# Kernel tuning notes

Hardware: AMD Instinct MI355X
Metric: run time of the kernel (lower is better)

## Reference

```python
import jax, jax.numpy as jnp
import numpy as np

B, S, HID = 2, 2048, 2048
NH, NKV, HD = 16, 8, 128
GROUPS = NH // NKV
EPS = 1e-6
SCALE = HD ** -0.5
ROPE_THETA = 1000000.0


def _rope_cos_sin(seq_len, head_dim, batch):
    inv_freq = 1.0 / (ROPE_THETA ** (np.arange(0, head_dim, 2, dtype=np.float32) / head_dim))
    t = np.arange(seq_len, dtype=np.float32)
    freqs = np.outer(t, inv_freq)                      # [S, HD/2]
    emb = np.concatenate([freqs, freqs], axis=-1)      # [S, HD]
    cos = np.broadcast_to(np.cos(emb), (batch, seq_len, head_dim))
    sin = np.broadcast_to(np.sin(emb), (batch, seq_len, head_dim))
    return jnp.asarray(cos), jnp.asarray(sin)


def setup_inputs() -> dict:
    key = jax.random.key(0)
    ks = jax.random.split(key, 6)
    hidden_states = jax.random.normal(ks[0], (B, S, HID), dtype=jnp.float32)
    cos, sin = _rope_cos_sin(S, HD, B)
    w_scale = HID ** -0.5
    Wq = jax.random.normal(ks[1], (NH * HD, HID), dtype=jnp.float32) * w_scale
    Wk = jax.random.normal(ks[2], (NKV * HD, HID), dtype=jnp.float32) * w_scale
    Wv = jax.random.normal(ks[3], (NKV * HD, HID), dtype=jnp.float32) * w_scale
    Wo = jax.random.normal(ks[4], (HID, NH * HD), dtype=jnp.float32) * w_scale
    q_norm_w = jnp.ones((HD,), dtype=jnp.float32)
    k_norm_w = jnp.ones((HD,), dtype=jnp.float32)
    return {"hidden_states": hidden_states, "cos": cos, "sin": sin,
            "Wq": Wq, "Wk": Wk, "Wv": Wv, "Wo": Wo,
            "q_norm_w": q_norm_w, "k_norm_w": k_norm_w}


def _rms_norm(x, w):
    # RMSNorm over last dim (head_dim), variance computed in fp32
    var = jnp.mean(x.astype(jnp.float32) ** 2, axis=-1, keepdims=True)
    return w * (x * jax.lax.rsqrt(var + EPS).astype(x.dtype))


def _rotate_half(x):
    x1, x2 = jnp.split(x, 2, axis=-1)
    return jnp.concatenate([-x2, x1], axis=-1)


def _apply_rope(x, cos, sin):
    # x: [B, H, S, D]; cos/sin: [B, S, D] -> unsqueeze head dim
    c = cos[:, None, :, :]
    s = sin[:, None, :, :]
    return x * c + _rotate_half(x) * s


def reference(hidden_states, cos, sin, Wq, Wk, Wv, Wo, q_norm_w, k_norm_w):
    b, s, _ = hidden_states.shape
    # QKV projections (bias=False per config.attention_bias)
    q = (hidden_states @ Wq.T).reshape(b, s, NH, HD)
    k = (hidden_states @ Wk.T).reshape(b, s, NKV, HD)
    v = (hidden_states @ Wv.T).reshape(b, s, NKV, HD)
    # Per-head QK RMSNorm, then [B, H, S, D]
    q = _rms_norm(q, q_norm_w).transpose(0, 2, 1, 3)
    k = _rms_norm(k, k_norm_w).transpose(0, 2, 1, 3)
    v = v.transpose(0, 2, 1, 3)
    # RoPE
    q = _apply_rope(q, cos, sin)
    k = _apply_rope(k, cos, sin)
    # GQA: expand kv heads to match query heads
    k = jnp.repeat(k, GROUPS, axis=1)
    v = jnp.repeat(v, GROUPS, axis=1)
    # SDPA (is_causal=False, mask=None, dropout=0)
    scores = jnp.einsum('bhqd,bhkd->bhqk', q, k) * SCALE
    probs = jax.nn.softmax(scores, axis=-1)
    attn = jnp.einsum('bhqk,bhkd->bhqd', probs, v)
    attn = attn.transpose(0, 2, 1, 3).reshape(b, s, NH * HD)
    return attn @ Wo.T
```

## Files before the change

kernel.cpp:

```cpp
#include <hip/hip_runtime.h>

using short8 = __attribute__((ext_vector_type(8))) short;
using f32x4  = __attribute__((ext_vector_type(4))) float;
using u32x2  = __attribute__((ext_vector_type(2))) unsigned int;
using u32x4  = __attribute__((ext_vector_type(4))) unsigned int;

#define MFMA16(a, b, c) __builtin_amdgcn_mfma_f32_16x16x32_bf16((a), (b), (c), 0, 0, 0)

__device__ inline float bf2f(ushort v) { return __uint_as_float(((unsigned int)v) << 16); }
__device__ inline unsigned int f2bfu(float f) {
  unsigned int u = __float_as_uint(f);
  return (u + 0x7fffu + ((u >> 16) & 1u)) >> 16;
}
__device__ inline unsigned int pk2(float a, float b) { return f2bfu(a) | (f2bfu(b) << 16); }
__device__ inline unsigned int pk2hw(float lo, float hi) {
  unsigned int r;
  asm("v_cvt_pk_bf16_f32 %0, %1, %2" : "=v"(r) : "v"(lo), "v"(hi));
  return r;
}

__device__ inline void gl_lds16(const ushort* g, ushort* l) {
  __builtin_amdgcn_global_load_lds(
      (const __attribute__((address_space(1))) void*)g,
      (__attribute__((address_space(3))) void*)l, 16, 0, 0);
}

__global__ __launch_bounds__(256) void f2b8(const float* __restrict__ src,
                                            ushort* __restrict__ dst, int n) {
  int i = (blockIdx.x * 256 + threadIdx.x) * 8;
  if (i >= n) return;
  f32x4 a = *(const f32x4*)(src + i);
  f32x4 b = *(const f32x4*)(src + i + 4);
  u32x4 o;
  o[0] = pk2(a[0], a[1]); o[1] = pk2(a[2], a[3]);
  o[2] = pk2(b[0], b[1]); o[3] = pk2(b[2], b[3]);
  *(u32x4*)(dst + i) = o;
}

__global__ __launch_bounds__(256) void wconv(const float* __restrict__ Wq,
                                             const float* __restrict__ Wk,
                                             const float* __restrict__ Wv,
                                             const float* __restrict__ Wo,
                                             ushort* __restrict__ Wcomb,
                                             ushort* __restrict__ Wob) {
  int blk = blockIdx.x;
  const float* src; ushort* dst; int off;
  if (blk < 2048)      { src = Wq; dst = Wcomb;           off = blk * 2048; }
  else if (blk < 3072) { src = Wk; dst = Wcomb + 4194304; off = (blk - 2048) * 2048; }
  else if (blk < 4096) { src = Wv; dst = Wcomb + 6291456; off = (blk - 3072) * 2048; }
  else                 { src = Wo; dst = Wob;             off = (blk - 4096) * 2048; }
  int i = off + threadIdx.x * 8;
  f32x4 a = *(const f32x4*)(src + i);
  f32x4 b = *(const f32x4*)(src + i + 4);
  u32x4 o;
  o[0] = pk2(a[0], a[1]); o[1] = pk2(a[2], a[3]);
  o[2] = pk2(b[0], b[1]); o[3] = pk2(b[2], b[3]);
  *(u32x4*)(dst + i) = o;
}

#define GPHASE(CB, P, STG, VMW)                                                     \
  {                                                                                 \
    if (P == 0) {                                                                   \
      _Pragma("unroll") for (int n = 0; n < 4; ++n) {                               \
        bf[n][0] = *(const short8*)&L[(CB)*32768 + bBase + n*1024 + rdoff];         \
        bf[n][1] = *(const short8*)&L[(CB)*32768 + bBase + n*1024 + (rdoff ^ 32)];  \
      }                                                                             \
    }                                                                               \
    short8 af[2][2];                                                                \
    _Pragma("unroll") for (int mi = 0; mi < 2; ++mi) {                              \
      af[mi][0] = *(const short8*)&L[(CB)*32768 + aBase + ((P)*2+mi)*1024 + rdoff];        \
      af[mi][1] = *(const short8*)&L[(CB)*32768 + aBase + ((P)*2+mi)*1024 + (rdoff ^ 32)]; \
    }                                                                               \
    STG;                                                                            \
    __builtin_amdgcn_s_barrier();                                                   \
    asm volatile("s_waitcnt lgkmcnt(0)" ::: "memory");                              \
    __builtin_amdgcn_s_setprio(1);                                                  \
    _Pragma("unroll") for (int mi = 0; mi < 2; ++mi)                                \
      _Pragma("unroll") for (int n = 0; n < 4; ++n) {                               \
        acc[(P)*2+mi][n] = MFMA16(af[mi][0], bf[n][0], acc[(P)*2+mi][n]);           \
        acc[(P)*2+mi][n] = MFMA16(af[mi][1], bf[n][1], acc[(P)*2+mi][n]);           \
      }                                                                             \
    __builtin_amdgcn_s_setprio(0);                                                  \
    VMW;                                                                            \
    __builtin_amdgcn_s_barrier();                                                   \
  }

#define VM4 asm volatile("s_waitcnt vmcnt(4)" ::: "memory")
#define NOPX (void)0

template <int OUTF32>
__global__ __launch_bounds__(512, 2) void gemm256(const ushort* __restrict__ A,
                                                  const ushort* __restrict__ B,
                                                  void* __restrict__ Cv,
                                                  int M, int N, int K) {
  __shared__ ushort L[65536];
  const int t = threadIdx.x;
  const int w = t >> 6, l = t & 63, lr = l & 15, lg = l >> 4;
  const int wr = w >> 2, wc = w & 3;
  const int m0 = blockIdx.x * 256, n0 = blockIdx.y * 256;
  const int NT = K >> 6, NI = NT >> 1;

  f32x4 acc[8][4] = {};

  const int rdoff = lr * 64 + ((lg ^ (lr & 7)) * 8);
  const int aBase = wr * 8192;
  const int bBase = 16384 + (wc >> 1) * 8192 + (wc & 1) * 4096;

  const int ch0 = w * 2, ch1 = w * 2 + 1;
  const int srow0 = ch0 * 8 + (l >> 3), srow1 = ch1 * 8 + (l >> 3);
  const int scol = ((l & 7) ^ (l >> 3)) * 8;

  auto stage_a = [&](int h, int kt, int cb) {
    int ktc = kt < NT ? kt : NT - 1;
    gl_lds16(A + (size_t)(m0 + h * 128 + srow0) * K + ktc * 64 + scol,
             (ushort*)&L[cb * 32768 + h * 8192 + ch0 * 512]);
    gl_lds16(A + (size_t)(m0 + h * 128 + srow1) * K + ktc * 64 + scol,
             (ushort*)&L[cb * 32768 + h * 8192 + ch1 * 512]);
  };
  auto stage_b = [&](int h, int kt, int cb) {
    int ktc = kt < NT ? kt : NT - 1;
    gl_lds16(B + (size_t)(n0 + h * 128 + srow0) * K + ktc * 64 + scol,
             (ushort*)&L[cb * 32768 + 16384 + h * 8192 + ch0 * 512]);
    gl_lds16(B + (size_t)(n0 + h * 128 + srow1) * K + ktc * 64 + scol,
             (ushort*)&L[cb * 32768 + 16384 + h * 8192 + ch1 * 512]);
  };

  stage_a(0, 0, 0); stage_a(1, 0, 0); stage_b(0, 0, 0); stage_b(1, 0, 0);
  stage_b(0, 1, 1); stage_b(1, 1, 1);
  VM4;
  __builtin_amdgcn_s_barrier();

  short8 bf[4][2];
  for (int I = 0; I < NI; ++I) {
    const int t1 = 2 * I + 1, t2 = 2 * I + 2, t3 = 2 * I + 3;
    GPHASE(0, 0, stage_a(0, t1, 1), NOPX)
    GPHASE(0, 1, stage_a(1, t1, 1), NOPX)
    GPHASE(0, 2, stage_b(0, t2, 0), NOPX)
    GPHASE(0, 3, stage_b(1, t2, 0), VM4)
    GPHASE(1, 0, stage_a(0, t2, 0), NOPX)
    GPHASE(1, 1, stage_a(1, t2, 0), NOPX)
    GPHASE(1, 2, stage_b(0, t3, 1), NOPX)
    GPHASE(1, 3, stage_b(1, t3, 1), VM4)
  }

  const int crow0 = m0 + wr * 128 + lg * 4;
  const int ccol = n0 + wc * 64 + lr;
  if (OUTF32) {
    float* C = (float*)Cv;
#pragma unroll
    for (int m = 0; m < 8; ++m)
#pragma unroll
      for (int n = 0; n < 4; ++n)
#pragma unroll
        for (int j = 0; j < 4; ++j)
          C[(size_t)(crow0 + m * 16 + j) * N + ccol + n * 16] = acc[m][n][j];
  } else {
    ushort* C = (ushort*)Cv;
#pragma unroll
    for (int m = 0; m < 8; ++m)
#pragma unroll
      for (int n = 0; n < 4; ++n)
#pragma unroll
        for (int j = 0; j < 4; ++j)
          C[(size_t)(crow0 + m * 16 + j) * N + ccol + n * 16] = (ushort)f2bfu(acc[m][n][j]);
  }
}

#define GP128(CB, P, STG, VMW)                                                      \
  {                                                                                 \
    if (P == 0) {                                                                   \
      _Pragma("unroll") for (int n = 0; n < 4; ++n) {                               \
        bf[n][0] = *(const short8*)&L[(CB)*24576 + bBase + n*1024 + rdoff];         \
        bf[n][1] = *(const short8*)&L[(CB)*24576 + bBase + n*1024 + (rdoff ^ 32)];  \
      }                                                                             \
    }                                                                               \
    short8 af0 = *(const short8*)&L[(CB)*24576 + aBase + (P)*1024 + rdoff];         \
    short8 af1 = *(const short8*)&L[(CB)*24576 + aBase + (P)*1024 + (rdoff ^ 32)];  \
    STG;                                                                            \
    __builtin_amdgcn_s_barrier();                                                   \
    asm volatile("s_waitcnt lgkmcnt(0)" ::: "memory");                              \
    __builtin_amdgcn_s_setprio(1);                                                  \
    _Pragma("unroll") for (int n = 0; n < 4; ++n) {                                 \
      acc[(P)][n] = MFMA16(af0, bf[n][0], acc[(P)][n]);                             \
      acc[(P)][n] = MFMA16(af1, bf[n][1], acc[(P)][n]);                             \
    }                                                                               \
    __builtin_amdgcn_s_setprio(0);                                                  \
    VMW;                                                                            \
    __builtin_amdgcn_s_barrier();                                                   \
  }

__global__ __launch_bounds__(512, 2) void gemm128(const ushort* __restrict__ A,
                                                  const ushort* __restrict__ B,
                                                  float* __restrict__ C,
                                                  int M, int N, int K) {
  __shared__ ushort L[49152];
  const int t = threadIdx.x;
  const int w = t >> 6, l = t & 63, lr = l & 15, lg = l >> 4;
  const int wr = w >> 2, wc = w & 3;
  const int m0 = blockIdx.x * 128, n0 = blockIdx.y * 256;
  const int NT = K >> 6, NI = NT >> 1;

  f32x4 acc[4][4] = {};

  const int rdoff = lr * 64 + ((lg ^ (lr & 7)) * 8);
  const int aBase = wr * 4096;
  const int bBase = 8192 + wc * 4096;
  const int scol = ((l & 7) ^ (l >> 3)) * 8;

  auto stage_a_h = [&](int h, int kt, int cb) {
    int ktc = kt < NT ? kt : NT - 1;
    int ch = h * 8 + w;
    gl_lds16(A + (size_t)(m0 + ch * 8 + (l >> 3)) * K + ktc * 64 + scol,
             (ushort*)&L[cb * 24576 + ch * 512]);
  };
  auto stage_b_h = [&](int h, int kt, int cb) {
    int ktc = kt < NT ? kt : NT - 1;
    int c0 = h * 16 + w * 2, c1 = c0 + 1;
    gl_lds16(B + (size_t)(n0 + c0 * 8 + (l >> 3)) * K + ktc * 64 + scol,
             (ushort*)&L[cb * 24576 + 8192 + c0 * 512]);
    gl_lds16(B + (size_t)(n0 + c1 * 8 + (l >> 3)) * K + ktc * 64 + scol,
             (ushort*)&L[cb * 24576 + 8192 + c1 * 512]);
  };

  stage_a_h(0, 0, 0); stage_a_h(1, 0, 0);
  stage_b_h(0, 0, 0); stage_b_h(1, 0, 0);
  stage_b_h(0, 1, 1); stage_b_h(1, 1, 1);
  VM4;
  __builtin_amdgcn_s_barrier();

  short8 bf[4][2];
  for (int I = 0; I < NI; ++I) {
    const int t1 = 2 * I + 1, t2 = 2 * I + 2, t3 = 2 * I + 3;
    GP128(0, 0, stage_a_h(0, t1, 1), NOPX)
    GP128(0, 1, stage_a_h(1, t1, 1), NOPX)
    GP128(0, 2, stage_b_h(0, t2, 0), NOPX)
    GP128(0, 3, stage_b_h(1, t2, 0), VM4)
    GP128(1, 0, stage_a_h(0, t2, 0), NOPX)
    GP128(1, 1, stage_a_h(1, t2, 0), NOPX)
    GP128(1, 2, stage_b_h(0, t3, 1), NOPX)
    GP128(1, 3, stage_b_h(1, t3, 1), VM4)
  }

  const int crow0 = m0 + wr * 64 + lg * 4;
  const int ccol = n0 + wc * 64 + lr;
#pragma unroll
  for (int m = 0; m < 4; ++m)
#pragma unroll
    for (int n = 0; n < 4; ++n)
#pragma unroll
      for (int j = 0; j < 4; ++j)
        C[(size_t)(crow0 + m * 16 + j) * N + ccol + n * 16] = acc[m][n][j];
}

__global__ __launch_bounds__(256) void qk_norm_rope(
    const ushort* __restrict__ QKVp, const float* __restrict__ cosb,
    const float* __restrict__ sinb, const float* __restrict__ qw,
    const float* __restrict__ kw, ushort* __restrict__ Qa, ushort* __restrict__ Ka) {
  int r = blockIdx.x * 4 + (threadIdx.x >> 6);
  int i = threadIdx.x & 63;
  int b, s, srccol;
  ushort* dst;
  const float* w;
  float scale;
  if (r < 65536) {
    b = r >> 15; int rem = r & 32767; s = rem >> 4; int h = rem & 15;
    srccol = h * 128;
    dst = Qa + ((size_t)((b * 16 + h) * 2048 + s)) * 128;
    w = qw;
    scale = 0.08838834764831845f * 1.4426950408889634f;
  } else {
    int rk = r - 65536;
    b = rk >> 14; int rem = rk & 16383; s = rem >> 3; int kvh = rem & 7;
    srccol = 2048 + kvh * 128;
    dst = Ka + ((size_t)((b * 8 + kvh) * 2048 + s)) * 128;
    w = kw;
    scale = 1.0f;
  }
  const ushort* src = QKVp + ((size_t)(b * 2048 + s)) * 4096 + srccol;
  float x0 = bf2f(src[i]), x1 = bf2f(src[i + 64]);
  float ss = x0 * x0 + x1 * x1;
#pragma unroll
  for (int m = 1; m < 64; m <<= 1) ss += __shfl_xor(ss, m);
  float inv = rsqrtf(ss * (1.0f / 128.0f) + 1e-6f);
  float xn0 = x0 * inv * w[i], xn1 = x1 * inv * w[i + 64];
  const float* cp = cosb + ((size_t)(b * 2048 + s)) * 128;
  const float* sp = sinb + ((size_t)(b * 2048 + s)) * 128;
  float o0 = (xn0 * cp[i] - xn1 * sp[i]) * scale;
  float o1 = (xn1 * cp[i + 64] + xn0 * sp[i + 64]) * scale;
  dst[i] = (ushort)f2bfu(o0);
  dst[i + 64] = (ushort)f2bfu(o1);
}

__global__ __launch_bounds__(256) void v_transpose(const ushort* __restrict__ QKVp,
                                                   ushort* __restrict__ Vt) {
  __shared__ ushort tile[64][136];
  int blk = blockIdx.x;
  int st = blk & 31, kvh = (blk >> 5) & 7, b = blk >> 8;
  int t = threadIdx.x;
  int s0 = st * 64;
  {
    int r = t >> 2, cseg = (t & 3) * 32;
    const ushort* src = QKVp + ((size_t)(b * 2048 + s0 + r)) * 4096 + 3072 + kvh * 128 + cseg;
#pragma unroll
    for (int i = 0; i < 4; ++i)
      *(uint4*)&tile[r][cseg + i * 8] = *(const uint4*)(src + i * 8);
  }
  __syncthreads();
  {
    int d = t >> 1, sh = (t & 1) * 32;
    ushort* dst = Vt + ((size_t)((b * 8 + kvh) * 128 + d)) * 2048 + s0 + sh;
    ushort buf[32];
#pragma unroll
    for (int k = 0; k < 32; ++k) buf[k] = tile[sh + k][d];
#pragma unroll
    for (int i = 0; i < 4; ++i) *(uint4*)(dst + i * 8) = *(uint4*)&buf[i * 8];
  }
}

__global__ __launch_bounds__(512, 4) void attn_kernel(const ushort* __restrict__ Qa,
                                                      const ushort* __restrict__ Ka,
                                                      const ushort* __restrict__ Vt,
                                                      ushort* __restrict__ Ctx) {
  __shared__ ushort Ks[2][64 * 128];
  __shared__ ushort Vs[2][128 * 64];
  __shared__ ushort Ps[8 * 1024];
  const int bh = blockIdx.x, b = bh >> 4, h = bh & 15, kvh = h >> 1;
  const int t = threadIdx.x, w = t >> 6, l = t & 63, lr = l & 15, lg = l >> 4;
  const int q0 = blockIdx.y * 128 + w * 16;
  const ushort* Qh = Qa + ((size_t)(b * 16 + h)) * 2048 * 128;
  const ushort* Kh = Ka + ((size_t)(b * 8 + kvh)) * 2048 * 128;
  const ushort* Vh = Vt + ((size_t)(b * 8 + kvh)) * 128 * 2048;

  short8 bq[4];
#pragma unroll
  for (int dc = 0; dc < 4; ++dc)
    bq[dc] = *(const short8*)&Qh[(size_t)(q0 + lr) * 128 + dc * 32 + lg * 8];
  asm volatile("s_waitcnt vmcnt(0)" ::: "memory");

  f32x4 accO[8] = {};
  float mrun = -3.0e38f, lrun = 0.f;

  auto stage = [&](int kt0, ushort* KSB, ushort* VSB) {
#pragma unroll
    for (int i = 0; i < 2; ++i) {
      const int c = w * 2 + i;
      const int krow = c * 4 + lg;
      gl_lds16(Kh + (size_t)(kt0 + krow) * 128 + ((lr ^ (krow & 7)) * 8), KSB + c * 512);
      const int vrow = c * 8 + (l >> 3);
      gl_lds16(Vh + (size_t)vrow * 2048 + kt0 + (((l & 7) ^ ((l >> 3) & 7)) * 8), VSB + c * 512);
    }
  };

  auto iter = [&](int kt, ushort* KSB, ushort* VSB) {
    f32x4 accS[4] = {};
    __builtin_amdgcn_s_setprio(1);
#pragma unroll
    for (int dc = 0; dc < 4; ++dc) {
      short8 ak[4];
#pragma unroll
      for (int kts = 0; kts < 4; ++kts)
        ak[kts] = *(const short8*)&KSB[(kts * 16 + lr) * 128 + ((dc * 4 + lg) ^ (lr & 7)) * 8];
#pragma unroll
      for (int kts = 0; kts < 4; ++kts)
        accS[kts] = MFMA16(ak[kts], bq[dc], accS[kts]);
    }
    __builtin_amdgcn_s_setprio(0);

    {
      float m0 = fmaxf(fmaxf(accS[0][0], accS[0][1]), fmaxf(accS[0][2], accS[0][3]));
      float m1 = fmaxf(fmaxf(accS[1][0], accS[1][1]), fmaxf(accS[1][2], accS[1][3]));
      float m2 = fmaxf(fmaxf(accS[2][0], accS[2][1]), fmaxf(accS[2][2], accS[2][3]));
      float m3 = fmaxf(fmaxf(accS[3][0], accS[3][1]), fmaxf(accS[3][2], accS[3][3]));
      float tm = fmaxf(fmaxf(m0, m1), fmaxf(m2, m3));
      tm = fmaxf(tm, __shfl_xor(tm, 16));
      tm = fmaxf(tm, __shfl_xor(tm, 32));
      if (!__all(tm <= mrun + 11.0f)) {
        float nm = fmaxf(mrun, tm);
        float cf = __builtin_amdgcn_exp2f(mrun - nm);
#pragma unroll
        for (int dc = 0; dc < 8; ++dc) {
          accO[dc][0] *= cf; accO[dc][1] *= cf;
          accO[dc][2] *= cf; accO[dc][3] *= cf;
        }
        lrun *= cf;
        mrun = nm;
      }
      float ts = 0.f;
#pragma unroll
      for (int kts = 0; kts < 4; ++kts)
#pragma unroll
        for (int j = 0; j < 4; ++j) {
          float p = __builtin_amdgcn_exp2f(accS[kts][j] - mrun);
          accS[kts][j] = p;
          ts += p;
        }
      ts += __shfl_xor(ts, 16);
      ts += __shfl_xor(ts, 32);
      lrun += ts;
#pragma unroll
      for (int kts = 0; kts < 4; ++kts) {
        u32x2 pv;
        pv[0] = pk2hw(accS[kts][0], accS[kts][1]);
        pv[1] = pk2hw(accS[kts][2], accS[kts][3]);
        *(u32x2*)&Ps[w * 1024 + lr * 64 +
                     (((kts * 2 + (lg >> 1)) ^ (lr & 7)) * 8 + (lg & 1) * 4)] = pv;
      }
    }
    asm volatile("s_waitcnt lgkmcnt(0)" ::: "memory");

    short8 bp[2];
#pragma unroll
    for (int ks = 0; ks < 2; ++ks)
      bp[ks] = *(const short8*)&Ps[w * 1024 + lr * 64 + ((ks * 4 + lg) ^ (lr & 7)) * 8];
    __builtin_amdgcn_s_setprio(1);
#pragma unroll
    for (int dc = 0; dc < 8; ++dc) {
      short8 av[2];
#pragma unroll
      for (int ks = 0; ks < 2; ++ks)
        av[ks] = *(const short8*)&VSB[(dc * 16 + lr) * 64 + ((ks * 4 + lg) ^ (lr & 7)) * 8];
#pragma unroll
      for (int ks = 0; ks < 2; ++ks)
        accO[dc] = MFMA16(av[ks], bp[ks], accO[dc]);
    }
    __builtin_amdgcn_s_setprio(0);

    asm volatile("" ::: "memory");
    __builtin_amdgcn_s_barrier();
    if (kt + 128 < 2048) {
      stage(kt + 128, KSB, VSB);
      asm volatile("s_waitcnt vmcnt(4)" ::: "memory");
    } else {
      asm volatile("s_waitcnt vmcnt(0)" ::: "memory");
    }
    __builtin_amdgcn_s_barrier();
  };

  stage(0, Ks[0], Vs[0]);
  stage(64, Ks[1], Vs[1]);
  asm volatile("s_waitcnt vmcnt(4)" ::: "memory");
  __builtin_amdgcn_s_barrier();

  for (int t2 = 0; t2 < 2048; t2 += 128) {
    iter(t2,      Ks[0], Vs[0]);
    iter(t2 + 64, Ks[1], Vs[1]);
  }

  {
    float inv = 1.0f / lrun;
    int srow = q0 + lr;
#pragma unroll
    for (int dc = 0; dc < 8; ++dc) {
      u32x2 ov;
      ov[0] = pk2hw(accO[dc][0] * inv, accO[dc][1] * inv);
      ov[1] = pk2hw(accO[dc][2] * inv, accO[dc][3] * inv);
      *(u32x2*)&Ctx[(size_t)(b * 2048 + srow) * 2048 + h * 128 + dc * 16 + lg * 4] = ov;
    }
  }
}

extern "C" void kernel_launch(void* const* d_in, const int* in_sizes, int n_in,
                              void* d_out, int out_size, void* d_ws, size_t ws_size,
                              hipStream_t stream) {
  const float* hidden = (const float*)d_in[0];
  const float* cosb   = (const float*)d_in[1];
  const float* sinb   = (const float*)d_in[2];
  const float* Wq     = (const float*)d_in[3];
  const float* Wk     = (const float*)d_in[4];
  const float* Wv     = (const float*)d_in[5];
  const float* Wo     = (const float*)d_in[6];
  const float* qw     = (const float*)d_in[7];
  const float* kw     = (const float*)d_in[8];

  char* ws = (char*)d_ws;
  ushort* Xb    = (ushort*)ws; ws += (size_t)4096 * 2048 * 2;
  ushort* Wcomb = (ushort*)ws; ws += (size_t)4096 * 2048 * 2;
  ushort* Wob   = (ushort*)ws; ws += (size_t)2048 * 2048 * 2;
  ushort* QKVp  = (ushort*)ws; ws += (size_t)4096 * 4096 * 2;
  ushort* Qa    = (ushort*)ws; ws += (size_t)2 * 16 * 2048 * 128 * 2;
  ushort* Ka    = (ushort*)ws; ws += (size_t)2 * 8 * 2048 * 128 * 2;
  ushort* Vt    = (ushort*)ws; ws += (size_t)2 * 8 * 2048 * 128 * 2;
  ushort* Ctx   = (ushort*)ws; ws += (size_t)4096 * 2048 * 2;

  f2b8<<<4096, 256, 0, stream>>>(hidden, Xb, 8388608);
  wconv<<<6144, 256, 0, stream>>>(Wq, Wk, Wv, Wo, Wcomb, Wob);

  gemm256<0><<<dim3(16, 16), 512, 0, stream>>>(Xb, Wcomb, (void*)QKVp, 4096, 4096, 2048);

  qk_norm_rope<<<24576, 256, 0, stream>>>(QKVp, cosb, sinb, qw, kw, Qa, Ka);
  v_transpose<<<512, 256, 0, stream>>>(QKVp, Vt);

  attn_kernel<<<dim3(32, 16), 512, 0, stream>>>(Qa, Ka, Vt, Ctx);

  gemm128<<<dim3(32, 8), 512, 0, stream>>>(Ctx, Wob, (float*)d_out, 4096, 2048, 2048);
}
```

Before: 358.8 us.

## Switch attention to 32x32x16 MFMA with register-resident P via permlane swap

```diff
diff --git a/kernel.cpp b/kernel.cpp
--- a/kernel.cpp
+++ b/kernel.cpp
@@ -2,10 +2,12 @@
 
 using short8 = __attribute__((ext_vector_type(8))) short;
 using f32x4  = __attribute__((ext_vector_type(4))) float;
+using f32x16 = __attribute__((ext_vector_type(16))) float;
 using u32x2  = __attribute__((ext_vector_type(2))) unsigned int;
 using u32x4  = __attribute__((ext_vector_type(4))) unsigned int;
 
 #define MFMA16(a, b, c) __builtin_amdgcn_mfma_f32_16x16x32_bf16((a), (b), (c), 0, 0, 0)
+#define MFMA32(a, b, c) __builtin_amdgcn_mfma_f32_32x32x16_bf16((a), (b), (c), 0, 0, 0)
 
 __device__ inline float bf2f(ushort v) { return __uint_as_float(((unsigned int)v) << 16); }
 __device__ inline unsigned int f2bfu(float f) {
@@ -317,119 +319,117 @@
   }
 }
 
-__global__ __launch_bounds__(512, 4) void attn_kernel(const ushort* __restrict__ Qa,
+#define MKFRAG(S, B, OUT)                                               \
+  {                                                                     \
+    unsigned pw0 = pk2hw(S[B + 0], S[B + 1]);                           \
+    unsigned pw1 = pk2hw(S[B + 2], S[B + 3]);                           \
+    unsigned pw2 = pk2hw(S[B + 4], S[B + 5]);                           \
+    unsigned pw3 = pk2hw(S[B + 6], S[B + 7]);                           \
+    asm("v_permlane32_swap_b32 %0, %1" : "+v"(pw0), "+v"(pw2));         \
+    asm("v_permlane32_swap_b32 %0, %1" : "+v"(pw1), "+v"(pw3));         \
+    union { unsigned u[4]; short8 s; } _r;                              \
+    _r.u[0] = pw0; _r.u[1] = pw1; _r.u[2] = pw2; _r.u[3] = pw3;         \
+    OUT = _r.s;                                                         \
+  }
+
+__global__ __launch_bounds__(256, 2) void attn_kernel(const ushort* __restrict__ Qa,
                                                       const ushort* __restrict__ Ka,
                                                       const ushort* __restrict__ Vt,
                                                       ushort* __restrict__ Ctx) {
   __shared__ ushort Ks[2][64 * 128];
   __shared__ ushort Vs[2][128 * 64];
-  __shared__ ushort Ps[8 * 1024];
+  __shared__ ushort Ot[4][32 * 40];
   const int bh = blockIdx.x, b = bh >> 4, h = bh & 15, kvh = h >> 1;
-  const int t = threadIdx.x, w = t >> 6, l = t & 63, lr = l & 15, lg = l >> 4;
-  const int q0 = blockIdx.y * 128 + w * 16;
+  const int t = threadIdx.x, w = t >> 6, l = t & 63;
+  const int q = l & 31, hi = l >> 5;
+  const int q0 = blockIdx.y * 128 + w * 32;
   const ushort* Qh = Qa + ((size_t)(b * 16 + h)) * 2048 * 128;
   const ushort* Kh = Ka + ((size_t)(b * 8 + kvh)) * 2048 * 128;
   const ushort* Vh = Vt + ((size_t)(b * 8 + kvh)) * 128 * 2048;
 
-  short8 bq[4];
-#pragma unroll
-  for (int dc = 0; dc < 4; ++dc)
-    bq[dc] = *(const short8*)&Qh[(size_t)(q0 + lr) * 128 + dc * 32 + lg * 8];
+  short8 qf[8];
+#pragma unroll
+  for (int dc = 0; dc < 8; ++dc)
+    qf[dc] = *(const short8*)&Qh[(size_t)(q0 + q) * 128 + dc * 16 + hi * 8];
   asm volatile("s_waitcnt vmcnt(0)" ::: "memory");
 
-  f32x4 accO[8] = {};
+  f32x16 accO[4] = {};
   float mrun = -3.0e38f, lrun = 0.f;
 
   auto stage = [&](int kt0, ushort* KSB, ushort* VSB) {
 #pragma unroll
-    for (int i = 0; i < 2; ++i) {
-      const int c = w * 2 + i;
-      const int krow = c * 4 + lg;
-      gl_lds16(Kh + (size_t)(kt0 + krow) * 128 + ((lr ^ (krow & 7)) * 8), KSB + c * 512);
-      const int vrow = c * 8 + (l >> 3);
-      gl_lds16(Vh + (size_t)vrow * 2048 + kt0 + (((l & 7) ^ ((l >> 3) & 7)) * 8), VSB + c * 512);
+    for (int i = 0; i < 4; ++i) {
+      const int krow = w * 16 + i * 4 + (l >> 4);
+      gl_lds16(Kh + (size_t)(kt0 + krow) * 128 + (((l & 15) ^ (krow & 15)) * 8),
+               KSB + (w * 16 + i * 4) * 128);
+      const int vrow = w * 32 + i * 8 + (l >> 3);
+      gl_lds16(Vh + (size_t)vrow * 2048 + kt0 + (((l & 7) ^ (vrow & 7)) * 8),
+               VSB + (w * 32 + i * 8) * 64);
     }
   };
 
   auto iter = [&](int kt, ushort* KSB, ushort* VSB) {
-    f32x4 accS[4] = {};
+    f32x16 s0 = {}, s1 = {};
     __builtin_amdgcn_s_setprio(1);
 #pragma unroll
-    for (int dc = 0; dc < 4; ++dc) {
-      short8 ak[4];
-#pragma unroll
-      for (int kts = 0; kts < 4; ++kts)
-        ak[kts] = *(const short8*)&KSB[(kts * 16 + lr) * 128 + ((dc * 4 + lg) ^ (lr & 7)) * 8];
-#pragma unroll
-      for (int kts = 0; kts < 4; ++kts)
-        accS[kts] = MFMA16(ak[kts], bq[dc], accS[kts]);
+    for (int dc = 0; dc < 8; ++dc) {
+      const int ksl = ((dc * 2 + hi) ^ (q & 15)) * 8;
+      short8 ak0 = *(const short8*)&KSB[q * 128 + ksl];
+      short8 ak1 = *(const short8*)&KSB[(32 + q) * 128 + ksl];
+      s0 = MFMA32(ak0, qf[dc], s0);
+      s1 = MFMA32(ak1, qf[dc], s1);
     }
     __builtin_amdgcn_s_setprio(0);
 
-    {
-      float m0 = fmaxf(fmaxf(accS[0][0], accS[0][1]), fmaxf(accS[0][2], accS[0][3]));
-      float m1 = fmaxf(fmaxf(accS[1][0], accS[1][1]), fmaxf(accS[1][2], accS[1][3]));
-      float m2 = fmaxf(fmaxf(accS[2][0], accS[2][1]), fmaxf(accS[2][2], accS[2][3]));
-      float m3 = fmaxf(fmaxf(accS[3][0], accS[3][1]), fmaxf(accS[3][2], accS[3][3]));
-      float tm = fmaxf(fmaxf(m0, m1), fmaxf(m2, m3));
-      tm = fmaxf(tm, __shfl_xor(tm, 16));
-      tm = fmaxf(tm, __shfl_xor(tm, 32));
-      if (!__all(tm <= mrun + 11.0f)) {
-        float nm = fmaxf(mrun, tm);
-        float cf = __builtin_amdgcn_exp2f(mrun - nm);
-#pragma unroll
-        for (int dc = 0; dc < 8; ++dc) {
-          accO[dc][0] *= cf; accO[dc][1] *= cf;
-          accO[dc][2] *= cf; accO[dc][3] *= cf;
-        }
-        lrun *= cf;
-        mrun = nm;
-      }
-      float ts = 0.f;
-#pragma unroll
-      for (int kts = 0; kts < 4; ++kts)
-#pragma unroll
-        for (int j = 0; j < 4; ++j) {
-          float p = __builtin_amdgcn_exp2f(accS[kts][j] - mrun);
-          accS[kts][j] = p;
-          ts += p;
-        }
-      ts += __shfl_xor(ts, 16);
-      ts += __shfl_xor(ts, 32);
-      lrun += ts;
-#pragma unroll
-      for (int kts = 0; kts < 4; ++kts) {
-        u32x2 pv;
-        pv[0] = pk2hw(accS[kts][0], accS[kts][1]);
-        pv[1] = pk2hw(accS[kts][2], accS[kts][3]);
-        *(u32x2*)&Ps[w * 1024 + lr * 64 +
-                     (((kts * 2 + (lg >> 1)) ^ (lr & 7)) * 8 + (lg & 1) * 4)] = pv;
-      }
-    }
-    asm volatile("s_waitcnt lgkmcnt(0)" ::: "memory");
-
-    short8 bp[2];
-#pragma unroll
-    for (int ks = 0; ks < 2; ++ks)
-      bp[ks] = *(const short8*)&Ps[w * 1024 + lr * 64 + ((ks * 4 + lg) ^ (lr & 7)) * 8];
+    float tm = -3.0e38f;
+#pragma unroll
+    for (int j = 0; j < 16; ++j) tm = fmaxf(tm, fmaxf(s0[j], s1[j]));
+    tm = fmaxf(tm, __shfl_xor(tm, 32));
+    if (!__all(tm <= mrun + 11.0f)) {
+      float nm = fmaxf(mrun, tm);
+      float cf = __builtin_amdgcn_exp2f(mrun - nm);
+#pragma unroll
+      for (int d0 = 0; d0 < 4; ++d0)
+#pragma unroll
+        for (int j = 0; j < 16; ++j) accO[d0][j] *= cf;
+      lrun *= cf;
+      mrun = nm;
+    }
+    float ts = 0.f;
+#pragma unroll
+    for (int j = 0; j < 16; ++j) {
+      float p0 = __builtin_amdgcn_exp2f(s0[j] - mrun);
+      float p1 = __builtin_amdgcn_exp2f(s1[j] - mrun);
+      s0[j] = p0; s1[j] = p1;
+      ts += p0 + p1;
+    }
+    ts += __shfl_xor(ts, 32);
+    lrun += ts;
+
+    short8 pf0, pf1, pf2, pf3;
+    MKFRAG(s0, 0, pf0) MKFRAG(s0, 8, pf1)
+    MKFRAG(s1, 0, pf2) MKFRAG(s1, 8, pf3)
+
     __builtin_amdgcn_s_setprio(1);
 #pragma unroll
-    for (int dc = 0; dc < 8; ++dc) {
-      short8 av[2];
-#pragma unroll
-      for (int ks = 0; ks < 2; ++ks)
-        av[ks] = *(const short8*)&VSB[(dc * 16 + lr) * 64 + ((ks * 4 + lg) ^ (lr & 7)) * 8];
-#pragma unroll
-      for (int ks = 0; ks < 2; ++ks)
-        accO[dc] = MFMA16(av[ks], bp[ks], accO[dc]);
+    for (int d0 = 0; d0 < 4; ++d0) {
+      const int vb = (d0 * 32 + q) * 64;
+      const int vx = q & 7;
+      short8 av0 = *(const short8*)&VSB[vb + ((0 + hi) ^ vx) * 8];
+      short8 av1 = *(const short8*)&VSB[vb + ((2 + hi) ^ vx) * 8];
+      short8 av2 = *(const short8*)&VSB[vb + ((4 + hi) ^ vx) * 8];
+      short8 av3 = *(const short8*)&VSB[vb + ((6 + hi) ^ vx) * 8];
+      accO[d0] = MFMA32(av0, pf0, accO[d0]);
+      accO[d0] = MFMA32(av1, pf1, accO[d0]);
+      accO[d0] = MFMA32(av2, pf2, accO[d0]);
+      accO[d0] = MFMA32(av3, pf3, accO[d0]);
     }
     __builtin_amdgcn_s_setprio(0);
 
-    asm volatile("" ::: "memory");
     __builtin_amdgcn_s_barrier();
     if (kt + 128 < 2048) {
       stage(kt + 128, KSB, VSB);
-      asm volatile("s_waitcnt vmcnt(4)" ::: "memory");
+      asm volatile("s_waitcnt vmcnt(8)" ::: "memory");
     } else {
       asm volatile("s_waitcnt vmcnt(0)" ::: "memory");
     }
@@ -438,7 +438,7 @@
 
   stage(0, Ks[0], Vs[0]);
   stage(64, Ks[1], Vs[1]);
-  asm volatile("s_waitcnt vmcnt(4)" ::: "memory");
+  asm volatile("s_waitcnt vmcnt(8)" ::: "memory");
   __builtin_amdgcn_s_barrier();
 
   for (int t2 = 0; t2 < 2048; t2 += 128) {
@@ -448,13 +448,22 @@
 
   {
     float inv = 1.0f / lrun;
-    int srow = q0 + lr;
-#pragma unroll
-    for (int dc = 0; dc < 8; ++dc) {
-      u32x2 ov;
-      ov[0] = pk2hw(accO[dc][0] * inv, accO[dc][1] * inv);
-      ov[1] = pk2hw(accO[dc][2] * inv, accO[dc][3] * inv);
-      *(u32x2*)&Ctx[(size_t)(b * 2048 + srow) * 2048 + h * 128 + dc * 16 + lg * 4] = ov;
+    ushort* ot = &Ot[w][0];
+    const int q2 = l >> 1;
+#pragma unroll
+    for (int d0 = 0; d0 < 4; ++d0) {
+#pragma unroll
+      for (int p = 0; p < 8; ++p) {
+        unsigned pw = pk2hw(accO[d0][2 * p] * inv, accO[d0][2 * p + 1] * inv);
+        const int dw = (p & 1) + 4 * (p >> 1) + 2 * hi;
+        *(unsigned*)&ot[q * 40 + dw * 2] = pw;
+      }
+#pragma unroll
+      for (int r = 0; r < 2; ++r) {
+        uint4 v = *(const uint4*)&ot[q2 * 40 + (l & 1) * 8 + r * 16];
+        *(uint4*)&Ctx[(size_t)(b * 2048 + q0 + q2) * 2048 + h * 128 + d0 * 32 +
+                      (l & 1) * 8 + r * 16] = v;
+      }
     }
   }
 }
@@ -490,7 +499,7 @@
   qk_norm_rope<<<24576, 256, 0, stream>>>(QKVp, cosb, sinb, qw, kw, Qa, Ka);
   v_transpose<<<512, 256, 0, stream>>>(QKVp, Vt);
 
-  attn_kernel<<<dim3(32, 16), 512, 0, stream>>>(Qa, Ka, Vt, Ctx);
+  attn_kernel<<<dim3(32, 16), 256, 0, stream>>>(Qa, Ka, Vt, Ctx);
 
   gemm128<<<dim3(32, 8), 512, 0, stream>>>(Ctx, Wob, (float*)d_out, 4096, 2048, 2048);
 }
```

Result: faster. 337.3 us (-6.0%).
